# Kernel tuning notes

Hardware: AMD Instinct MI355X
Metric: run time of the kernel (lower is better)

The kernel has to match this reference:

```python
import jax, jax.numpy as jnp
import numpy as np

N = 50000          # nodes
E = 1_600_000      # edges
H = 64             # agg_hidden (heads=1, concat)
IN = 7             # in_channels
EDIM = 4           # edge_dim
G = 256            # num graphs in batch
FC = 128           # fc_hidden
NC = 2             # num_classes
SLOPE = 0.2        # GATv2 LeakyReLU negative slope


def setup_inputs() -> dict:
    key = jax.random.key(0)
    ks = jax.random.split(key, 24)
    s = 0.1
    d = {
        "x": jax.random.normal(ks[0], (N, IN), dtype=jnp.float32),
        "edge_index": jax.random.randint(ks[1], (2, E), 0, N, dtype=jnp.int32),
        "edge_attr": jax.random.normal(ks[2], (E, EDIM), dtype=jnp.float32),
        "batch": jnp.sort(jax.random.randint(ks[3], (N,), 0, G, dtype=jnp.int32)),
        # GATv2 layer 0 (in=7 -> 64)
        "Wl0": jax.random.normal(ks[4], (IN, H)) * s,
        "bl0": jnp.zeros((H,), jnp.float32),
        "Wr0": jax.random.normal(ks[5], (IN, H)) * s,
        "br0": jnp.zeros((H,), jnp.float32),
        "We0": jax.random.normal(ks[6], (EDIM, H)) * s,
        "att0": jax.random.normal(ks[7], (H,)) * s,
        "bias0": jnp.zeros((H,), jnp.float32),
        # GATv2 layer 1 (64 -> 64)
        "Wl1": jax.random.normal(ks[8], (H, H)) * s,
        "bl1": jnp.zeros((H,), jnp.float32),
        "Wr1": jax.random.normal(ks[9], (H, H)) * s,
        "br1": jnp.zeros((H,), jnp.float32),
        "We1": jax.random.normal(ks[10], (EDIM, H)) * s,
        "att1": jax.random.normal(ks[11], (H,)) * s,
        "bias1": jnp.zeros((H,), jnp.float32),
        # MLP head
        "fc1_w": jax.random.normal(ks[12], (H, FC)) * s,
        "fc1_b": jnp.zeros((FC,), jnp.float32),
        "fc2_w": jax.random.normal(ks[13], (FC, NC)) * s,
        "fc2_b": jnp.zeros((NC,), jnp.float32),
    }
    return d


def _gatv2(x, src, dst, edge_attr, Wl, bl, Wr, br, We, att, bias):
    # GATv2Conv (heads=1, concat=True, edge_dim=EDIM), eval mode (no dropout)
    xl = x @ Wl + bl                         # source-side projection [N,H]
    xr = x @ Wr + br                         # target-side projection [N,H]
    e = xl[src] + xr[dst] + edge_attr @ We   # per-edge pre-activation [E,H]
    score = jax.nn.leaky_relu(e, SLOPE) @ att  # [E]
    # segment softmax over destination nodes
    m = jax.ops.segment_max(score, dst, num_segments=N)
    ex = jnp.exp(score - m[dst])
    den = jax.ops.segment_sum(ex, dst, num_segments=N)
    alpha = ex / (den[dst] + 1e-16)
    out = jax.ops.segment_sum(xl[src] * alpha[:, None], dst, num_segments=N)
    return out + bias


def reference(x, edge_index, edge_attr, batch,
              Wl0, bl0, Wr0, br0, We0, att0, bias0,
              Wl1, bl1, Wr1, br1, We1, att1, bias1,
              fc1_w, fc1_b, fc2_w, fc2_b):
    src, dst = edge_index[0], edge_index[1]
    h = jax.nn.elu(_gatv2(x, src, dst, edge_attr, Wl0, bl0, Wr0, br0, We0, att0, bias0))
    h = jax.nn.elu(_gatv2(h, src, dst, edge_attr, Wl1, bl1, Wr1, br1, We1, att1, bias1))
    # global mean pool over graphs
    sums = jax.ops.segment_sum(h, batch, num_segments=G)
    cnt = jax.ops.segment_sum(jnp.ones((h.shape[0],), h.dtype), batch, num_segments=G)
    g = sums / jnp.maximum(cnt, 1.0)[:, None]      # [G,H]
    g = jax.nn.relu(g @ fc1_w + fc1_b)
    logits = g @ fc2_w + fc2_b
    return jax.nn.log_softmax(logits, axis=1)
```

## Files before the change

### kernel.cpp

```cpp
#include <hip/hip_runtime.h>
#include <hip/hip_fp16.h>

#define N_NODES 50000
#define N_EDGES 1600000
#define H 64
#define IN_CH 7
#define EDIM 4
#define G_GRAPHS 256
#define FC 128
#define NC 2
#define SLOPE 0.2f
#define NBUCK 196
#define EPB1 8192
#define NB1 ((N_EDGES + EPB1 - 1) / EPB1)
#define PAIR_BLOCKS ((N_NODES * 32 + 255) / 256)

typedef _Float16 h2v __attribute__((ext_vector_type(2)));

__device__ __forceinline__ float fdot2f(h2v a, h2v b, float c) {
#if defined(__has_builtin) && __has_builtin(__builtin_amdgcn_fdot2)
    return __builtin_amdgcn_fdot2(a, b, c, false);
#else
    return c + (float)a[0] * (float)b[0] + (float)a[1] * (float)b[1];
#endif
}

__device__ __forceinline__ float wave_sum_to63(float x) {
    x += __int_as_float(__builtin_amdgcn_update_dpp(0, __float_as_int(x), 0x111, 0xf, 0xf, true));
    x += __int_as_float(__builtin_amdgcn_update_dpp(0, __float_as_int(x), 0x112, 0xf, 0xf, true));
    x += __int_as_float(__builtin_amdgcn_update_dpp(0, __float_as_int(x), 0x114, 0xf, 0xf, true));
    x += __int_as_float(__builtin_amdgcn_update_dpp(0, __float_as_int(x), 0x118, 0xf, 0xf, true));
    x += __int_as_float(__builtin_amdgcn_update_dpp(0, __float_as_int(x), 0x142, 0xf, 0xf, true));
    x += __int_as_float(__builtin_amdgcn_update_dpp(0, __float_as_int(x), 0x143, 0xf, 0xf, true));
    return x;
}
__device__ __forceinline__ float lane63_bcast(float x) {
    return __int_as_float(__builtin_amdgcn_readlane(__float_as_int(x), 63));
}
__device__ __forceinline__ float readlane_f(float x, int i) {
    return __int_as_float(__builtin_amdgcn_readlane(__float_as_int(x), i));
}

__global__ __launch_bounds__(256) void front_kernel(
        const int* __restrict__ dst, int* __restrict__ rank1, int* __restrict__ bhist,
        const float* __restrict__ xin,
        const float* __restrict__ Wl0, const float* __restrict__ bl0,
        const float* __restrict__ Wr0, const float* __restrict__ br0,
        __half2* __restrict__ xlh, __half2* __restrict__ xrh,
        const float* __restrict__ We0, const float* __restrict__ We1,
        const float* __restrict__ Wl1, const float* __restrict__ bl1,
        const float* __restrict__ Wr1, const float* __restrict__ br1,
        __half2* __restrict__ weh0, __half2* __restrict__ weh1,
        __half2* __restrict__ wt, float* __restrict__ bb,
        const float* __restrict__ att0, const float* __restrict__ att1,
        __half2* __restrict__ atth0, __half2* __restrict__ atth1) {
    __shared__ int hist[NBUCK];
    int b = blockIdx.x;
    int t = threadIdx.x;
    if (b < NB1) {
        if (t < NBUCK) hist[t] = 0;
        __syncthreads();
#pragma unroll
        for (int i = 0; i < EPB1 / 256; ++i) {
            int e = b * EPB1 + i * 256 + t;
            if (e < N_EDGES) {
                int k = dst[e] >> 8;
                rank1[e] = atomicAdd(&hist[k], 1);
            }
        }
        __syncthreads();
        if (t < NBUCK) bhist[b * NBUCK + t] = hist[t];
    } else if (b < NB1 + PAIR_BLOCKS) {
        int idx = (b - NB1) * 256 + t;
        if (idx < N_NODES * 32) {
            int n = idx >> 5;
            int c = idx & 31;
            const float* xi = xin + n * IN_CH;
            float2 bl2 = ((const float2*)bl0)[c];
            float2 br2 = ((const float2*)br0)[c];
            float al0 = bl2.x, al1 = bl2.y, ar0 = br2.x, ar1 = br2.y;
#pragma unroll
            for (int k = 0; k < IN_CH; ++k) {
                float xv = xi[k];
                float2 wl2 = ((const float2*)(Wl0 + k * H))[c];
                float2 wr2 = ((const float2*)(Wr0 + k * H))[c];
                al0 += xv * wl2.x; al1 += xv * wl2.y;
                ar0 += xv * wr2.x; ar1 += xv * wr2.y;
            }
            xlh[idx] = __floats2half2_rn(al0, al1);
            xrh[idx] = __floats2half2_rn(ar0, ar1);
        }
    } else {
        if (t < 32) {
            for (int k = 0; k < 4; ++k)
                weh0[t * 4 + k] = __floats2half2_rn(We0[k * H + 2 * t], We0[k * H + 2 * t + 1]);
        } else if (t < 64) {
            int c = t - 32;
            for (int k = 0; k < 4; ++k)
                weh1[c * 4 + k] = __floats2half2_rn(We1[k * H + 2 * c], We1[k * H + 2 * c + 1]);
        }
        if (t < 128) {
            const float* W = (t < 64) ? Wl1 : Wr1;
            int c = t & 63;
            for (int kk = 0; kk < 32; ++kk)
                wt[t * 32 + kk] = __floats2half2_rn(W[(2 * kk) * H + c], W[(2 * kk + 1) * H + c]);
            bb[t] = (t < 64) ? bl1[c] : br1[c];
        } else if (t < 160) {
            int c = t - 128;
            atth0[c] = __floats2half2_rn(att0[2 * c], att0[2 * c + 1]);
            atth1[c] = __floats2half2_rn(att1[2 * c], att1[2 * c + 1]);
        }
    }
}

__global__ __launch_bounds__(256) void bucket_scan_kernel(
        const int* __restrict__ bhist, int* __restrict__ bases, int* __restrict__ cb_start) {
    __shared__ int lds[256];
    int t = threadIdx.x;
    int run = 0;
    if (t < NBUCK) {
        for (int b = 0; b < NB1; ++b) {
            bases[b * NBUCK + t] = run;
            run += bhist[b * NBUCK + t];
        }
    }
    lds[t] = (t < NBUCK) ? run : 0;
    __syncthreads();
    for (int off = 1; off < 256; off <<= 1) {
        int x = (t >= off) ? lds[t - off] : 0;
        __syncthreads();
        lds[t] += x;
        __syncthreads();
    }
    if (t < NBUCK) cb_start[t] = lds[t] - run;
    if (t == NBUCK - 1) cb_start[NBUCK] = lds[t];
}

__global__ void coarse_scatter_kernel(const int* __restrict__ src, const int* __restrict__ dst,
                                      const int* __restrict__ rank1, const int* __restrict__ bases,
                                      const int* __restrict__ cb_start,
                                      const float* __restrict__ edge_attr,
                                      int4* __restrict__ tmp) {
    int e = blockIdx.x * blockDim.x + threadIdx.x;
    if (e >= N_EDGES) return;
    int d = dst[e];
    int k = d >> 8;
    int b = e / EPB1;
    int slot = cb_start[k] + bases[b * NBUCK + k] + rank1[e];
    float4 ea = ((const float4*)edge_attr)[e];
    __half2 h01 = __floats2half2_rn(ea.x, ea.y);
    __half2 h23 = __floats2half2_rn(ea.z, ea.w);
    int4 ent;
    ent.x = src[e];
    ent.y = *reinterpret_cast<int*>(&h01);
    ent.z = *reinterpret_cast<int*>(&h23);
    ent.w = d;
    tmp[slot] = ent;
}

__global__ __launch_bounds__(256) void fine_sort_kernel(
        const int* __restrict__ cb_start, const int4* __restrict__ tmp,
        int4* __restrict__ csr, int* __restrict__ row_start) {
    __shared__ int hist2[256];
    __shared__ int cursor[256];
    __shared__ int lds[256];
    int k = blockIdx.x;
    int t = threadIdx.x;
    int beg = cb_start[k], end = cb_start[k + 1];
    hist2[t] = 0;
    __syncthreads();
    for (int i = beg + t; i < end; i += 256)
        atomicAdd(&hist2[tmp[i].w & 255], 1);
    __syncthreads();
    int v = hist2[t];
    lds[t] = v;
    __syncthreads();
    for (int off = 1; off < 256; off <<= 1) {
        int x = (t >= off) ? lds[t - off] : 0;
        __syncthreads();
        lds[t] += x;
        __syncthreads();
    }
    int pre = lds[t] - v;
    cursor[t] = pre;
    int node = k * 256 + t;
    if (node <= N_NODES) row_start[node] = beg + pre;
    __syncthreads();
    for (int i = beg + t; i < end; i += 256) {
        int4 ent = tmp[i];
        int slot = beg + atomicAdd(&cursor[ent.w & 255], 1);
        csr[slot] = ent;
    }
}

__global__ __launch_bounds__(256) void proj1_kernel(
        const float* __restrict__ xin,
        const __half2* __restrict__ wt,
        const float* __restrict__ bb,
        __half2* __restrict__ xlh, __half2* __restrict__ xrh) {
    int g = __builtin_amdgcn_readfirstlane((int)(threadIdx.x >> 6));
    int lane = threadIdx.x & 63;
    int node = blockIdx.x * 64 + lane;
    if (node >= N_NODES) return;

    h2v xrow[32];
    const float4* xp = (const float4*)(xin + node * 64);
#pragma unroll
    for (int q = 0; q < 16; ++q) {
        float4 v = xp[q];
        __half2 a = __floats2half2_rn(v.x, v.y);
        __half2 b = __floats2half2_rn(v.z, v.w);
        xrow[2 * q]     = *reinterpret_cast<h2v*>(&a);
        xrow[2 * q + 1] = *reinterpret_cast<h2v*>(&b);
    }

    __half2* outp = (g < 2) ? xlh : xrh;
    int chbase = g * 32;
    int localbase = (g & 1) * 16;

#pragma unroll
    for (int cp = 0; cp < 16; ++cp) {
        int ch0 = chbase + 2 * cp;
        const h2v* w0 = (const h2v*)(wt + ch0 * 32);
        const h2v* w1 = (const h2v*)(wt + (ch0 + 1) * 32);
        float a0 = bb[ch0], a1 = bb[ch0 + 1];
#pragma unroll
        for (int kk = 0; kk < 32; ++kk) {
            a0 = fdot2f(xrow[kk], w0[kk], a0);
            a1 = fdot2f(xrow[kk], w1[kk], a1);
        }
        outp[node * 32 + localbase + cp] = __floats2half2_rn(a0, a1);
    }
}

__global__ __launch_bounds__(256) void fused_agg_kernel(
        const int* __restrict__ row_start,
        const int4* __restrict__ csr,
        const __half2* __restrict__ xlh, const __half2* __restrict__ xrh,
        const __half2* __restrict__ weh, const __half2* __restrict__ atth,
        const float* __restrict__ bias,
        float* __restrict__ out) {
    int wave = (blockIdx.x * blockDim.x + threadIdx.x) >> 6;
    if (wave >= N_NODES) return;
    int lane = threadIdx.x & 63;
    int c = lane & 31;
    int hb = lane >> 5;
    int d = wave;
    int beg = __builtin_amdgcn_readfirstlane(row_start[d]);
    int end = __builtin_amdgcn_readfirstlane(row_start[d + 1]);

    const h2v sl = { (_Float16)SLOPE, (_Float16)SLOPE };
    const int4* xb = (const int4*)(xrh + (size_t)d * 32);

    float l_lane = 0.f;
    float ax0 = 0.f, ay0 = 0.f, ax1 = 0.f, ay1 = 0.f;

    for (int cbeg = beg; cbeg < end; cbeg += 64) {
        int n = end - cbeg;
        int nn = min(n, 64);

        int idx = cbeg + lane;
        idx = idx < end ? idx : end - 1;
        int4 ent = csr[idx];
        __half2 ea01 = *reinterpret_cast<__half2*>(&ent.y);
        __half2 ea23 = *reinterpret_cast<__half2*>(&ent.z);
        __half2 e0 = __half2half2(__low2half(ea01));
        __half2 e1 = __half2half2(__high2half(ea01));
        __half2 e2 = __half2half2(__low2half(ea23));
        __half2 e3 = __half2half2(__high2half(ea23));
        const int4* xa = (const int4*)(xlh + (size_t)ent.x * 32);
        float acc0 = 0.f, acc1 = 0.f;
#pragma unroll
        for (int k = 0; k < 8; ++k) {
            int4 va = xa[k];
            int4 vb = xb[k];
            const __half2* ha = reinterpret_cast<const __half2*>(&va);
            const __half2* hc = reinterpret_cast<const __half2*>(&vb);
#pragma unroll
            for (int j = 0; j < 4; ++j) {
                int cc = k * 4 + j;
                __half2 v2 = __hadd2(ha[j], hc[j]);
                v2 = __hfma2(e0, weh[cc * 4 + 0], v2);
                v2 = __hfma2(e1, weh[cc * 4 + 1], v2);
                v2 = __hfma2(e2, weh[cc * 4 + 2], v2);
                v2 = __hfma2(e3, weh[cc * 4 + 3], v2);
                h2v vv = *reinterpret_cast<h2v*>(&v2);
                h2v Lv = __builtin_elementwise_max(vv, sl * vv);
                __half2 av = atth[cc];
                if (j & 1)
                    acc1 = fdot2f(Lv, *reinterpret_cast<h2v*>(&av), acc1);
                else
                    acc0 = fdot2f(Lv, *reinterpret_cast<h2v*>(&av), acc0);
            }
        }
        float p = __expf(acc0 + acc1);
        p = (lane < n) ? p : 0.f;
        l_lane += p;
        int esrc = ent.x;

        int j = 0;
        for (; j + 4 <= nn; j += 4) {
            int sA0 = __builtin_amdgcn_readlane(esrc, j + 0);
            int sB0 = __builtin_amdgcn_readlane(esrc, j + 1);
            int sA1 = __builtin_amdgcn_readlane(esrc, j + 2);
            int sB1 = __builtin_amdgcn_readlane(esrc, j + 3);
            float pA0 = readlane_f(p, j + 0), pB0 = readlane_f(p, j + 1);
            float pA1 = readlane_f(p, j + 2), pB1 = readlane_f(p, j + 3);
            int s0 = hb ? sB0 : sA0;
            int s1 = hb ? sB1 : sA1;
            float pv0 = hb ? pB0 : pA0;
            float pv1 = hb ? pB1 : pA1;
            float2 x0 = __half22float2(xlh[s0 * 32 + c]);
            float2 x1 = __half22float2(xlh[s1 * 32 + c]);
            ax0 += pv0 * x0.x; ay0 += pv0 * x0.y;
            ax1 += pv1 * x1.x; ay1 += pv1 * x1.y;
        }
        for (; j + 2 <= nn; j += 2) {
            int sA = __builtin_amdgcn_readlane(esrc, j + 0);
            int sB = __builtin_amdgcn_readlane(esrc, j + 1);
            float pA = readlane_f(p, j + 0), pB = readlane_f(p, j + 1);
            int s = hb ? sB : sA;
            float pv = hb ? pB : pA;
            float2 xf = __half22float2(xlh[s * 32 + c]);
            ax0 += pv * xf.x; ay0 += pv * xf.y;
        }
        if (j < nn) {
            int sA = __builtin_amdgcn_readlane(esrc, j);
            float pA = readlane_f(p, j);
            float pv = hb ? 0.f : pA;
            float2 xf = __half22float2(xlh[sA * 32 + c]);
            ax0 += pv * xf.x; ay0 += pv * xf.y;
        }
    }

    float l = lane63_bcast(wave_sum_to63(l_lane));
    float accx = ax0 + ax1, accy = ay0 + ay1;
    accx += __shfl_xor(accx, 32, 64);
    accy += __shfl_xor(accy, 32, 64);
    if (hb == 0) {
        float inv = 1.f / (l + 1e-16f);
        float2 b2 = ((const float2*)bias)[c];
        float o0 = accx * inv + b2.x;
        float o1 = accy * inv + b2.y;
        o0 = o0 > 0.f ? o0 : expm1f(o0);
        o1 = o1 > 0.f ? o1 : expm1f(o1);
        ((float2*)out)[d * 32 + c] = float2{o0, o1};
    }
}

__global__ __launch_bounds__(256) void pool_head_kernel(
        const float* __restrict__ h, const int* __restrict__ batch,
        const float* __restrict__ fc1w, const float* __restrict__ fc1b,
        const float* __restrict__ fc2w, const float* __restrict__ fc2b,
        float* __restrict__ out) {
    int g = blockIdx.x;
    int lo = 0, hi = N_NODES;
    while (lo < hi) { int mid = (lo + hi) >> 1; if (batch[mid] < g) lo = mid + 1; else hi = mid; }
    int start = lo;
    hi = N_NODES;
    while (lo < hi) { int mid = (lo + hi) >> 1; if (batch[mid] < g + 1) lo = mid + 1; else hi = mid; }
    int end = lo;

    int lane = threadIdx.x & 63;
    int w = threadIdx.x >> 6;
    float s = 0.f;
    for (int n = start + w; n < end; n += 4) s += h[n * H + lane];
    __shared__ float red[4][H];
    __shared__ float gv[H];
    __shared__ float f[FC];
    __shared__ float lg[NC];
    red[w][lane] = s;
    __syncthreads();
    if (w == 0) {
        float tot = red[0][lane] + red[1][lane] + red[2][lane] + red[3][lane];
        gv[lane] = tot / fmaxf((float)(end - start), 1.f);
    }
    __syncthreads();
    int t = threadIdx.x;
    if (t < FC) {
        float acc = fc1b[t];
#pragma unroll 16
        for (int k = 0; k < H; ++k) acc += gv[k] * fc1w[k * FC + t];
        f[t] = fmaxf(acc, 0.f);
    }
    __syncthreads();
    if (t < NC) {
        float a = fc2b[t];
        for (int k = 0; k < FC; ++k) a += f[k] * fc2w[k * NC + t];
        lg[t] = a;
    }
    __syncthreads();
    if (t < NC) {
        float mx = fmaxf(lg[0], lg[1]);
        float lse = mx + logf(expf(lg[0] - mx) + expf(lg[1] - mx));
        out[g * NC + t] = lg[t] - lse;
    }
}

extern "C" void kernel_launch(void* const* d_in, const int* in_sizes, int n_in,
                              void* d_out, int out_size, void* d_ws, size_t ws_size,
                              hipStream_t stream) {
    const float* x         = (const float*)d_in[0];
    const int*   edge_idx  = (const int*)d_in[1];
    const float* edge_attr = (const float*)d_in[2];
    const int*   batch     = (const int*)d_in[3];
    const float* Wl0  = (const float*)d_in[4];
    const float* bl0  = (const float*)d_in[5];
    const float* Wr0  = (const float*)d_in[6];
    const float* br0  = (const float*)d_in[7];
    const float* We0  = (const float*)d_in[8];
    const float* att0 = (const float*)d_in[9];
    const float* bias0= (const float*)d_in[10];
    const float* Wl1  = (const float*)d_in[11];
    const float* bl1  = (const float*)d_in[12];
    const float* Wr1  = (const float*)d_in[13];
    const float* br1  = (const float*)d_in[14];
    const float* We1  = (const float*)d_in[15];
    const float* att1 = (const float*)d_in[16];
    const float* bias1= (const float*)d_in[17];
    const float* fc1w = (const float*)d_in[18];
    const float* fc1b = (const float*)d_in[19];
    const float* fc2w = (const float*)d_in[20];
    const float* fc2b = (const float*)d_in[21];

    const int NH = N_NODES * H;
    __half2* xlh    = (__half2*)d_ws;
    __half2* xrh    = xlh + N_NODES * 32;
    float* C        = (float*)(xrh + N_NODES * 32);
    float* escore   = C + NH;
    float* pad      = escore + N_EDGES;
    int4*  tmp      = (int4*)C;
    int4*  csr      = (int4*)(pad + N_EDGES);
    int*   srcs     = (int*)(csr + N_EDGES);
    int*   row_start= srcs + N_EDGES;
    unsigned* m_enc = (unsigned*)(row_start + N_NODES + 1);
    int*   rank1    = (int*)(m_enc + N_NODES);
    int*   bhist    = rank1 + N_EDGES;
    int*   bases    = bhist + NB1 * NBUCK;
    int*   cb_start = bases + NB1 * NBUCK;
    __half2* weh0   = (__half2*)(cb_start + NBUCK + 1);
    __half2* weh1   = weh0 + 128;
    __half2* wt1    = weh1 + 128;
    float* bb1      = (float*)(wt1 + 128 * 32);
    __half2* atth0  = (__half2*)(bb1 + 128);
    __half2* atth1  = atth0 + 32;

    const int* src = edge_idx;
    const int* dst = edge_idx + N_EDGES;

    const int edgeBlocks = (N_EDGES + 255) / 256;
    const int waveBlocks = (N_NODES * 64 + 255) / 256;
    const int p1Blocks   = (N_NODES + 63) / 64;
    const int frontBlocks = NB1 + PAIR_BLOCKS + 1;

    front_kernel<<<frontBlocks, 256, 0, stream>>>(dst, rank1, bhist,
                                                  x, Wl0, bl0, Wr0, br0, xlh, xrh,
                                                  We0, We1, Wl1, bl1, Wr1, br1,
                                                  weh0, weh1, wt1, bb1,
                                                  att0, att1, atth0, atth1);
    bucket_scan_kernel<<<1, 256, 0, stream>>>(bhist, bases, cb_start);
    coarse_scatter_kernel<<<edgeBlocks, 256, 0, stream>>>(src, dst, rank1, bases, cb_start,
                                                          edge_attr, tmp);
    fine_sort_kernel<<<NBUCK, 256, 0, stream>>>(cb_start, tmp, csr, row_start);

    fused_agg_kernel<<<waveBlocks, 256, 0, stream>>>(row_start, csr, xlh, xrh,
                                                     weh0, atth0, bias0, C);

    proj1_kernel<<<p1Blocks, 256, 0, stream>>>(C, wt1, bb1, xlh, xrh);
    fused_agg_kernel<<<waveBlocks, 256, 0, stream>>>(row_start, csr, xlh, xrh,
                                                     weh1, atth1, bias1, C);

    pool_head_kernel<<<G_GRAPHS, 256, 0, stream>>>(C, batch, fc1w, fc1b, fc2w, fc2b, (float*)d_out);
}
```

Baseline: 450.3 us.

## Replace two-level CSR sort with 32-node buckets and LDS-atomic aggregation

```diff
diff --git a/kernel.cpp b/kernel.cpp
--- a/kernel.cpp
+++ b/kernel.cpp
@@ -10,7 +10,10 @@
 #define FC 128
 #define NC 2
 #define SLOPE 0.2f
-#define NBUCK 196
+#define BSH 5
+#define BNODES 32
+#define NBUCK ((N_NODES + BNODES - 1) / BNODES)
+#define ACC_STRIDE 65
 #define EPB1 8192
 #define NB1 ((N_EDGES + EPB1 - 1) / EPB1)
 #define PAIR_BLOCKS ((N_NODES * 32 + 255) / 256)
@@ -25,24 +28,8 @@
 #endif
 }
 
-__device__ __forceinline__ float wave_sum_to63(float x) {
-    x += __int_as_float(__builtin_amdgcn_update_dpp(0, __float_as_int(x), 0x111, 0xf, 0xf, true));
-    x += __int_as_float(__builtin_amdgcn_update_dpp(0, __float_as_int(x), 0x112, 0xf, 0xf, true));
-    x += __int_as_float(__builtin_amdgcn_update_dpp(0, __float_as_int(x), 0x114, 0xf, 0xf, true));
-    x += __int_as_float(__builtin_amdgcn_update_dpp(0, __float_as_int(x), 0x118, 0xf, 0xf, true));
-    x += __int_as_float(__builtin_amdgcn_update_dpp(0, __float_as_int(x), 0x142, 0xf, 0xf, true));
-    x += __int_as_float(__builtin_amdgcn_update_dpp(0, __float_as_int(x), 0x143, 0xf, 0xf, true));
-    return x;
-}
-__device__ __forceinline__ float lane63_bcast(float x) {
-    return __int_as_float(__builtin_amdgcn_readlane(__float_as_int(x), 63));
-}
-__device__ __forceinline__ float readlane_f(float x, int i) {
-    return __int_as_float(__builtin_amdgcn_readlane(__float_as_int(x), i));
-}
-
 __global__ __launch_bounds__(256) void front_kernel(
-        const int* __restrict__ dst, int* __restrict__ rank1, int* __restrict__ bhist,
+        const int* __restrict__ dst, int* __restrict__ rank1, int* __restrict__ bcnt,
         const float* __restrict__ xin,
         const float* __restrict__ Wl0, const float* __restrict__ bl0,
         const float* __restrict__ Wr0, const float* __restrict__ br0,
@@ -54,22 +41,17 @@
         __half2* __restrict__ wt, float* __restrict__ bb,
         const float* __restrict__ att0, const float* __restrict__ att1,
         __half2* __restrict__ atth0, __half2* __restrict__ atth1) {
-    __shared__ int hist[NBUCK];
     int b = blockIdx.x;
     int t = threadIdx.x;
     if (b < NB1) {
-        if (t < NBUCK) hist[t] = 0;
-        __syncthreads();
 #pragma unroll
         for (int i = 0; i < EPB1 / 256; ++i) {
             int e = b * EPB1 + i * 256 + t;
             if (e < N_EDGES) {
-                int k = dst[e] >> 8;
-                rank1[e] = atomicAdd(&hist[k], 1);
+                int k = dst[e] >> BSH;
+                rank1[e] = atomicAdd(&bcnt[k], 1);
             }
         }
-        __syncthreads();
-        if (t < NBUCK) bhist[b * NBUCK + t] = hist[t];
     } else if (b < NB1 + PAIR_BLOCKS) {
         int idx = (b - NB1) * 256 + t;
         if (idx < N_NODES * 32) {
@@ -113,40 +95,42 @@
     }
 }
 
-__global__ __launch_bounds__(256) void bucket_scan_kernel(
-        const int* __restrict__ bhist, int* __restrict__ bases, int* __restrict__ cb_start) {
+__global__ __launch_bounds__(256) void cb_scan_kernel(
+        const int* __restrict__ bcnt, int* __restrict__ cb_start) {
     __shared__ int lds[256];
+    __shared__ int carry_s;
     int t = threadIdx.x;
-    int run = 0;
-    if (t < NBUCK) {
-        for (int b = 0; b < NB1; ++b) {
-            bases[b * NBUCK + t] = run;
-            run += bhist[b * NBUCK + t];
-        }
-    }
-    lds[t] = (t < NBUCK) ? run : 0;
-    __syncthreads();
-    for (int off = 1; off < 256; off <<= 1) {
-        int x = (t >= off) ? lds[t - off] : 0;
+    if (t == 0) carry_s = 0;
+    __syncthreads();
+    for (int base = 0; base < NBUCK; base += 256) {
+        int v = (base + t < NBUCK) ? bcnt[base + t] : 0;
+        lds[t] = v;
         __syncthreads();
-        lds[t] += x;
+        for (int off = 1; off < 256; off <<= 1) {
+            int x = (t >= off) ? lds[t - off] : 0;
+            __syncthreads();
+            lds[t] += x;
+            __syncthreads();
+        }
+        int carry = carry_s;
+        if (base + t < NBUCK) cb_start[base + t] = carry + lds[t] - v;
         __syncthreads();
-    }
-    if (t < NBUCK) cb_start[t] = lds[t] - run;
-    if (t == NBUCK - 1) cb_start[NBUCK] = lds[t];
+        if (t == 255) carry_s = carry + lds[255];
+        __syncthreads();
+    }
+    if (t == 0) cb_start[NBUCK] = carry_s;
 }
 
 __global__ void coarse_scatter_kernel(const int* __restrict__ src, const int* __restrict__ dst,
-                                      const int* __restrict__ rank1, const int* __restrict__ bases,
+                                      const int* __restrict__ rank1,
                                       const int* __restrict__ cb_start,
                                       const float* __restrict__ edge_attr,
                                       int4* __restrict__ tmp) {
     int e = blockIdx.x * blockDim.x + threadIdx.x;
     if (e >= N_EDGES) return;
     int d = dst[e];
-    int k = d >> 8;
-    int b = e / EPB1;
-    int slot = cb_start[k] + bases[b * NBUCK + k] + rank1[e];
+    int k = d >> BSH;
+    int slot = cb_start[k] + rank1[e];
     float4 ea = ((const float4*)edge_attr)[e];
     __half2 h01 = __floats2half2_rn(ea.x, ea.y);
     __half2 h23 = __floats2half2_rn(ea.z, ea.w);
@@ -158,41 +142,6 @@
     tmp[slot] = ent;
 }
 
-__global__ __launch_bounds__(256) void fine_sort_kernel(
-        const int* __restrict__ cb_start, const int4* __restrict__ tmp,
-        int4* __restrict__ csr, int* __restrict__ row_start) {
-    __shared__ int hist2[256];
-    __shared__ int cursor[256];
-    __shared__ int lds[256];
-    int k = blockIdx.x;
-    int t = threadIdx.x;
-    int beg = cb_start[k], end = cb_start[k + 1];
-    hist2[t] = 0;
-    __syncthreads();
-    for (int i = beg + t; i < end; i += 256)
-        atomicAdd(&hist2[tmp[i].w & 255], 1);
-    __syncthreads();
-    int v = hist2[t];
-    lds[t] = v;
-    __syncthreads();
-    for (int off = 1; off < 256; off <<= 1) {
-        int x = (t >= off) ? lds[t - off] : 0;
-        __syncthreads();
-        lds[t] += x;
-        __syncthreads();
-    }
-    int pre = lds[t] - v;
-    cursor[t] = pre;
-    int node = k * 256 + t;
-    if (node <= N_NODES) row_start[node] = beg + pre;
-    __syncthreads();
-    for (int i = beg + t; i < end; i += 256) {
-        int4 ent = tmp[i];
-        int slot = beg + atomicAdd(&cursor[ent.w & 255], 1);
-        csr[slot] = ent;
-    }
-}
-
 __global__ __launch_bounds__(256) void proj1_kernel(
         const float* __restrict__ xin,
         const __half2* __restrict__ wt,
@@ -233,35 +182,24 @@
     }
 }
 
-__global__ __launch_bounds__(256) void fused_agg_kernel(
-        const int* __restrict__ row_start,
-        const int4* __restrict__ csr,
+__global__ __launch_bounds__(256) void gat_bucket_kernel(
+        const int* __restrict__ cb_start, const int4* __restrict__ tmp,
         const __half2* __restrict__ xlh, const __half2* __restrict__ xrh,
         const __half2* __restrict__ weh, const __half2* __restrict__ atth,
-        const float* __restrict__ bias,
-        float* __restrict__ out) {
-    int wave = (blockIdx.x * blockDim.x + threadIdx.x) >> 6;
-    if (wave >= N_NODES) return;
-    int lane = threadIdx.x & 63;
-    int c = lane & 31;
-    int hb = lane >> 5;
-    int d = wave;
-    int beg = __builtin_amdgcn_readfirstlane(row_start[d]);
-    int end = __builtin_amdgcn_readfirstlane(row_start[d + 1]);
-
+        const float* __restrict__ bias, float* __restrict__ out) {
+    __shared__ float acc[BNODES * ACC_STRIDE];
+    int k = blockIdx.x;
+    int t = threadIdx.x;
+    int nb = k << BSH;
+    for (int i = t; i < BNODES * ACC_STRIDE; i += 256) acc[i] = 0.f;
+    __syncthreads();
+
+    int beg = cb_start[k], end = cb_start[k + 1];
+    int lane = t & 63;
     const h2v sl = { (_Float16)SLOPE, (_Float16)SLOPE };
-    const int4* xb = (const int4*)(xrh + (size_t)d * 32);
-
-    float l_lane = 0.f;
-    float ax0 = 0.f, ay0 = 0.f, ax1 = 0.f, ay1 = 0.f;
-
-    for (int cbeg = beg; cbeg < end; cbeg += 64) {
-        int n = end - cbeg;
-        int nn = min(n, 64);
-
-        int idx = cbeg + lane;
-        idx = idx < end ? idx : end - 1;
-        int4 ent = csr[idx];
+
+    for (int i = beg + t; i < end; i += 256) {
+        int4 ent = tmp[i];
         __half2 ea01 = *reinterpret_cast<__half2*>(&ent.y);
         __half2 ea23 = *reinterpret_cast<__half2*>(&ent.z);
         __half2 e0 = __half2half2(__low2half(ea01));
@@ -269,16 +207,18 @@
         __half2 e2 = __half2half2(__low2half(ea23));
         __half2 e3 = __half2half2(__high2half(ea23));
         const int4* xa = (const int4*)(xlh + (size_t)ent.x * 32);
+        const int4* xb = (const int4*)(xrh + (size_t)ent.w * 32);
+        int4 va[8];
         float acc0 = 0.f, acc1 = 0.f;
 #pragma unroll
-        for (int k = 0; k < 8; ++k) {
-            int4 va = xa[k];
-            int4 vb = xb[k];
-            const __half2* ha = reinterpret_cast<const __half2*>(&va);
+        for (int kk = 0; kk < 8; ++kk) {
+            va[kk] = xa[kk];
+            int4 vb = xb[kk];
+            const __half2* ha = reinterpret_cast<const __half2*>(&va[kk]);
             const __half2* hc = reinterpret_cast<const __half2*>(&vb);
 #pragma unroll
             for (int j = 0; j < 4; ++j) {
-                int cc = k * 4 + j;
+                int cc = kk * 4 + j;
                 __half2 v2 = __hadd2(ha[j], hc[j]);
                 v2 = __hfma2(e0, weh[cc * 4 + 0], v2);
                 v2 = __hfma2(e1, weh[cc * 4 + 1], v2);
@@ -294,57 +234,32 @@
             }
         }
         float p = __expf(acc0 + acc1);
-        p = (lane < n) ? p : 0.f;
-        l_lane += p;
-        int esrc = ent.x;
-
-        int j = 0;
-        for (; j + 4 <= nn; j += 4) {
-            int sA0 = __builtin_amdgcn_readlane(esrc, j + 0);
-            int sB0 = __builtin_amdgcn_readlane(esrc, j + 1);
-            int sA1 = __builtin_amdgcn_readlane(esrc, j + 2);
-            int sB1 = __builtin_amdgcn_readlane(esrc, j + 3);
-            float pA0 = readlane_f(p, j + 0), pB0 = readlane_f(p, j + 1);
-            float pA1 = readlane_f(p, j + 2), pB1 = readlane_f(p, j + 3);
-            int s0 = hb ? sB0 : sA0;
-            int s1 = hb ? sB1 : sA1;
-            float pv0 = hb ? pB0 : pA0;
-            float pv1 = hb ? pB1 : pA1;
-            float2 x0 = __half22float2(xlh[s0 * 32 + c]);
-            float2 x1 = __half22float2(xlh[s1 * 32 + c]);
-            ax0 += pv0 * x0.x; ay0 += pv0 * x0.y;
-            ax1 += pv1 * x1.x; ay1 += pv1 * x1.y;
-        }
-        for (; j + 2 <= nn; j += 2) {
-            int sA = __builtin_amdgcn_readlane(esrc, j + 0);
-            int sB = __builtin_amdgcn_readlane(esrc, j + 1);
-            float pA = readlane_f(p, j + 0), pB = readlane_f(p, j + 1);
-            int s = hb ? sB : sA;
-            float pv = hb ? pB : pA;
-            float2 xf = __half22float2(xlh[s * 32 + c]);
-            ax0 += pv * xf.x; ay0 += pv * xf.y;
-        }
-        if (j < nn) {
-            int sA = __builtin_amdgcn_readlane(esrc, j);
-            float pA = readlane_f(p, j);
-            float pv = hb ? 0.f : pA;
-            float2 xf = __half22float2(xlh[sA * 32 + c]);
-            ax0 += pv * xf.x; ay0 += pv * xf.y;
-        }
-    }
-
-    float l = lane63_bcast(wave_sum_to63(l_lane));
-    float accx = ax0 + ax1, accy = ay0 + ay1;
-    accx += __shfl_xor(accx, 32, 64);
-    accy += __shfl_xor(accy, 32, 64);
-    if (hb == 0) {
+        int dl = ent.w - nb;
+        float* ab = acc + dl * ACC_STRIDE;
+        atomicAdd(ab + 64, p);
+        const __half2* rowh = reinterpret_cast<const __half2*>(va);
+#pragma unroll 8
+        for (int s = 0; s < 32; ++s) {
+            int cp = (lane + s) & 31;
+            float2 xf = __half22float2(rowh[cp]);
+            atomicAdd(ab + 2 * cp,     p * xf.x);
+            atomicAdd(ab + 2 * cp + 1, p * xf.y);
+        }
+    }
+    __syncthreads();
+
+    for (int idx = t; idx < BNODES * 32; idx += 256) {
+        int n = idx >> 5, cp = idx & 31;
+        int node = nb + n;
+        if (node >= N_NODES) continue;
+        float l = acc[n * ACC_STRIDE + 64];
         float inv = 1.f / (l + 1e-16f);
-        float2 b2 = ((const float2*)bias)[c];
-        float o0 = accx * inv + b2.x;
-        float o1 = accy * inv + b2.y;
+        float2 b2 = ((const float2*)bias)[cp];
+        float o0 = acc[n * ACC_STRIDE + 2 * cp]     * inv + b2.x;
+        float o1 = acc[n * ACC_STRIDE + 2 * cp + 1] * inv + b2.y;
         o0 = o0 > 0.f ? o0 : expm1f(o0);
         o1 = o1 > 0.f ? o1 : expm1f(o1);
-        ((float2*)out)[d * 32 + c] = float2{o0, o1};
+        ((float2*)out)[node * 32 + cp] = float2{o0, o1};
     }
 }
 
@@ -423,21 +338,13 @@
     const float* fc2w = (const float*)d_in[20];
     const float* fc2b = (const float*)d_in[21];
 
-    const int NH = N_NODES * H;
     __half2* xlh    = (__half2*)d_ws;
     __half2* xrh    = xlh + N_NODES * 32;
     float* C        = (float*)(xrh + N_NODES * 32);
-    float* escore   = C + NH;
-    float* pad      = escore + N_EDGES;
-    int4*  tmp      = (int4*)C;
-    int4*  csr      = (int4*)(pad + N_EDGES);
-    int*   srcs     = (int*)(csr + N_EDGES);
-    int*   row_start= srcs + N_EDGES;
-    unsigned* m_enc = (unsigned*)(row_start + N_NODES + 1);
-    int*   rank1    = (int*)(m_enc + N_NODES);
-    int*   bhist    = rank1 + N_EDGES;
-    int*   bases    = bhist + NB1 * NBUCK;
-    int*   cb_start = bases + NB1 * NBUCK;
+    int4*  tmp      = (int4*)(C + N_NODES * 64);
+    int*   rank1    = (int*)(tmp + N_EDGES);
+    int*   bcnt     = rank1 + N_EDGES;
+    int*   cb_start = bcnt + NBUCK;
     __half2* weh0   = (__half2*)(cb_start + NBUCK + 1);
     __half2* weh1   = weh0 + 128;
     __half2* wt1    = weh1 + 128;
@@ -449,26 +356,25 @@
     const int* dst = edge_idx + N_EDGES;
 
     const int edgeBlocks = (N_EDGES + 255) / 256;
-    const int waveBlocks = (N_NODES * 64 + 255) / 256;
     const int p1Blocks   = (N_NODES + 63) / 64;
     const int frontBlocks = NB1 + PAIR_BLOCKS + 1;
 
-    front_kernel<<<frontBlocks, 256, 0, stream>>>(dst, rank1, bhist,
+    hipMemsetAsync(bcnt, 0, NBUCK * sizeof(int), stream);
+    front_kernel<<<frontBlocks, 256, 0, stream>>>(dst, rank1, bcnt,
                                                   x, Wl0, bl0, Wr0, br0, xlh, xrh,
                                                   We0, We1, Wl1, bl1, Wr1, br1,
                                                   weh0, weh1, wt1, bb1,
                                                   att0, att1, atth0, atth1);
-    bucket_scan_kernel<<<1, 256, 0, stream>>>(bhist, bases, cb_start);
-    coarse_scatter_kernel<<<edgeBlocks, 256, 0, stream>>>(src, dst, rank1, bases, cb_start,
+    cb_scan_kernel<<<1, 256, 0, stream>>>(bcnt, cb_start);
+    coarse_scatter_kernel<<<edgeBlocks, 256, 0, stream>>>(src, dst, rank1, cb_start,
                                                           edge_attr, tmp);
-    fine_sort_kernel<<<NBUCK, 256, 0, stream>>>(cb_start, tmp, csr, row_start);
-
-    fused_agg_kernel<<<waveBlocks, 256, 0, stream>>>(row_start, csr, xlh, xrh,
-                                                     weh0, atth0, bias0, C);
+
+    gat_bucket_kernel<<<NBUCK, 256, 0, stream>>>(cb_start, tmp, xlh, xrh,
+                                                 weh0, atth0, bias0, C);
 
     proj1_kernel<<<p1Blocks, 256, 0, stream>>>(C, wt1, bb1, xlh, xrh);
-    fused_agg_kernel<<<waveBlocks, 256, 0, stream>>>(row_start, csr, xlh, xrh,
-                                                     weh1, atth1, bias1, C);
+    gat_bucket_kernel<<<NBUCK, 256, 0, stream>>>(cb_start, tmp, xlh, xrh,
+                                                 weh1, atth1, bias1, C);
 
     pool_head_kernel<<<G_GRAPHS, 256, 0, stream>>>(C, batch, fc1w, fc1b, fc2w, fc2b, (float*)d_out);
 }
```

Result: slower. 1.658 ms (+268.2%).
